# Kernel tuning notes

Measured on AMD Instinct MI355X. Metric: run time of the kernel, lower is better.

## Reference

```python
import jax, jax.numpy as jnp
import numpy as np

B, T, D = 4, 2048, 1024
H = 16
DH = D // H

def setup_inputs() -> dict:
    key = jax.random.key(0)
    k1, k2, k3 = jax.random.split(key, 3)
    x = jax.random.normal(k1, (B, T, D), dtype=jnp.float32)
    causal_mask = jnp.tril(jnp.ones((T, T), dtype=bool))[None, None]  # (1,1,T,T)
    Wqkv = jax.random.normal(k2, (D, 3 * D), dtype=jnp.float32) * (1.0 / np.sqrt(D))
    Wout = jax.random.normal(k3, (D, D), dtype=jnp.float32) * (1.0 / np.sqrt(D))
    return {"x": x, "causal_mask": causal_mask, "Wqkv": Wqkv, "Wout": Wout}

def reference(x, causal_mask, Wqkv, Wout):
    Bb, Tt, C = x.shape
    scale = jnp.sqrt(jnp.asarray(DH, dtype=x.dtype))
    qkv = x @ Wqkv                                   # (B,T,3D)
    qkv = qkv.reshape(Bb, Tt, 3, H, DH)
    qkv = jnp.transpose(qkv, (2, 0, 3, 1, 4))        # (3,B,H,T,DH)
    q, k, v = qkv[0], qkv[1], qkv[2]
    attn = jnp.einsum('bhqd,bhkd->bhqk', q, k) / scale
    attn = jnp.where(causal_mask, attn, jnp.asarray(-jnp.inf, dtype=attn.dtype))
    attn = jax.nn.softmax(attn, axis=-1)             # dropout p=0 -> identity
    out = jnp.einsum('bhqk,bhkd->bhqd', attn, v)     # (B,H,T,DH)
    out = jnp.transpose(out, (0, 2, 1, 3)).reshape(Bb, Tt, C)
    return out @ Wout
```

## Files before the change

kernel.cpp:

```cpp
#include <hip/hip_runtime.h>
#include <hip/hip_bf16.h>
#include <math.h>


#define Bb 4
#define Tt 2048
#define Dd 1024
#define Hh 16
#define DH 64
#define Mrows (Bb*Tt)
#define NEGBIG (-1.0e30f)
#define KB64 (Dd/64)
#define CHUNKS 1024
#define TILEU16 8192

typedef unsigned short u16;
typedef __attribute__((ext_vector_type(8))) short bf16x8;
typedef __attribute__((ext_vector_type(4))) float f32x4;

__device__ __forceinline__ u16 f2bf(float f) {
    union { float f; unsigned int i; } v; v.f = f;
    unsigned int x = v.i;
    return (u16)((x + 0x7fffu + ((x >> 16) & 1u)) >> 16);
}

__device__ __forceinline__ unsigned int cvt_pk_bf16(float lo, float hi) {
    unsigned int r;
    asm("v_cvt_pk_bf16_f32 %0, %1, %2" : "=v"(r) : "v"(lo), "v"(hi));
    return r;
}

__device__ __forceinline__ float exp2_(float x) {
#if __has_builtin(__builtin_amdgcn_exp2f)
    return __builtin_amdgcn_exp2f(x);
#else
    return __expf(x * 0.69314718056f);
#endif
}

typedef __attribute__((address_space(1))) const void glob_cv;
typedef __attribute__((address_space(3))) void lds_v;
__device__ __forceinline__ void gl2lds16(const void* g, void* l) {
    __builtin_amdgcn_global_load_lds((glob_cv*)g, (lds_v*)l, 16, 0, 0);
}

__global__ __launch_bounds__(256) void convert_x_tiled(const float* __restrict__ src,
                                                       u16* __restrict__ dst) {
    const int mb = blockIdx.x >> 4, kb = blockIdx.x & 15;
    const int row = threadIdx.x & 127, half = threadIdx.x >> 7;
    const float* s = src + (size_t)(mb * 128 + row) * Dd + kb * 64 + half * 32;
    u16* base = dst + (size_t)blockIdx.x * TILEU16;
    #pragma unroll
    for (int cq = 0; cq < 4; ++cq) {
        const int kq = half * 4 + cq;
        float4 f0 = *(const float4*)(s + cq * 8);
        float4 f1 = *(const float4*)(s + cq * 8 + 4);
        uint4 o;
        o.x = cvt_pk_bf16(f0.x, f0.y); o.y = cvt_pk_bf16(f0.z, f0.w);
        o.z = cvt_pk_bf16(f1.x, f1.y); o.w = cvt_pk_bf16(f1.z, f1.w);
        *(uint4*)(base + (size_t)(kq * 128 + row) * 8) = o;
    }
}

__global__ __launch_bounds__(256) void convert_w_tiled(const float* __restrict__ W,
                                                       u16* __restrict__ Wt,
                                                       int N) {
    __shared__ u16 t[128][68];
    const int nb = blockIdx.x, kb = blockIdx.y;
    const int k0 = kb * 64, n0 = nb * 128;
    const int k = threadIdx.x >> 2, ng = threadIdx.x & 3;
    const float* s = W + (size_t)(k0 + k) * N + n0 + ng * 32;
    #pragma unroll
    for (int i = 0; i < 8; ++i) {
        float4 f = *(const float4*)(s + i * 4);
        const int n = ng * 32 + i * 4;
        t[n + 0][k] = f2bf(f.x); t[n + 1][k] = f2bf(f.y);
        t[n + 2][k] = f2bf(f.z); t[n + 3][k] = f2bf(f.w);
    }
    __syncthreads();
    u16* base = Wt + (size_t)(nb * KB64 + kb) * TILEU16;
    #pragma unroll
    for (int it = 0; it < 4; ++it) {
        const int c = it * 256 + threadIdx.x;
        const int row = c & 127, kq = c >> 7;
        union { u16 u[8]; uint4 v; } o;
        #pragma unroll
        for (int j = 0; j < 8; ++j) o.u[j] = t[row][kq * 8 + j];
        *(uint4*)(base + (size_t)c * 8) = o.v;
    }
}

template <int MODE>
__global__ __launch_bounds__(256) void gemm_mfma(const u16* __restrict__ At,
                                                 const u16* __restrict__ Bt,
                                                 u16* __restrict__ Qo,
                                                 u16* __restrict__ KT,
                                                 u16* __restrict__ VtT,
                                                 float* __restrict__ Out) {
    __shared__ u16 As[8 * 128 * 8];
    __shared__ u16 Bs[8 * 128 * 8];
    const int tid  = threadIdx.x;
    const int lane = tid & 63, w = tid >> 6;
    const int ml   = lane & 15, q = lane >> 4;
    const int wm   = w >> 1, wn = w & 1;
    const int m0 = blockIdx.y * 128;

    const u16* Abase = At + (size_t)blockIdx.y * KB64 * TILEU16;
    const u16* Bbase = Bt + (size_t)blockIdx.x * KB64 * TILEU16;

    f32x4 acc[4][4];
    #pragma unroll
    for (int i = 0; i < 4; ++i)
        #pragma unroll
        for (int j = 0; j < 4; ++j) acc[i][j] = (f32x4){0.f, 0.f, 0.f, 0.f};

    for (int kb = 0; kb < KB64; ++kb) {
        __syncthreads();
        const u16* Ak = Abase + (size_t)kb * TILEU16;
        const u16* Bk = Bbase + (size_t)kb * TILEU16;
        #pragma unroll
        for (int it = 0; it < 4; ++it) {
            const int c = it * 256 + tid;
            gl2lds16(Ak + (size_t)c * 8, (char*)As + c * 16);
            gl2lds16(Bk + (size_t)c * 8, (char*)Bs + c * 16);
        }
        __syncthreads();

        #pragma unroll
        for (int ks = 0; ks < 2; ++ks) {
            const int kq = ks * 4 + q;
            bf16x8 af[4], bfr[4];
            #pragma unroll
            for (int i = 0; i < 4; ++i)
                af[i] = *(const bf16x8*)((const char*)As +
                        ((kq * 128) + wm * 64 + i * 16 + ml) * 16);
            #pragma unroll
            for (int j = 0; j < 4; ++j)
                bfr[j] = *(const bf16x8*)((const char*)Bs +
                        ((kq * 128) + wn * 64 + j * 16 + ml) * 16);
            #pragma unroll
            for (int i = 0; i < 4; ++i)
                #pragma unroll
                for (int j = 0; j < 4; ++j)
                    acc[i][j] = __builtin_amdgcn_mfma_f32_16x16x32_bf16(
                            bfr[j], af[i], acc[i][j], 0, 0, 0);
        }
    }

    if (MODE == 0) {
        const int s  = (blockIdx.x * 128) >> 10;
        const int h0 = ((blockIdx.x * 128) & 1023) >> 6;
        #pragma unroll
        for (int i = 0; i < 4; ++i) {
            const int m  = m0 + wm * 64 + i * 16 + ml;
            const int bb = m >> 11, t = m & 2047;
            const int bhn = bb * Hh + h0 + wn;
            #pragma unroll
            for (int j = 0; j < 4; ++j) {
                const int dh = j * 16 + q * 4;
                if (s == 2) {
                    u16* vb = VtT + (size_t)(bhn * 16 + (t >> 7)) * TILEU16;
                    #pragma unroll
                    for (int r = 0; r < 4; ++r)
                        vb[(size_t)(((t >> 3) & 15) * 64 + dh + r) * 8 + (t & 7)]
                            = f2bf(acc[i][j][r]);
                } else if (s == 1) {
                    uint2 pk;
                    pk.x = cvt_pk_bf16(acc[i][j][0], acc[i][j][1]);
                    pk.y = cvt_pk_bf16(acc[i][j][2], acc[i][j][3]);
                    *(uint2*)(KT + (size_t)(bhn * 16 + (t >> 7)) * TILEU16 +
                              (size_t)((j * 2 + (q >> 1)) * 128 + (t & 127)) * 8 +
                              (q & 1) * 4) = pk;
                } else {
                    const float sc = 0.125f * 1.44269504089f;
                    uint2 pk;
                    pk.x = cvt_pk_bf16(acc[i][j][0] * sc, acc[i][j][1] * sc);
                    pk.y = cvt_pk_bf16(acc[i][j][2] * sc, acc[i][j][3] * sc);
                    *(uint2*)(Qo + ((size_t)bhn * Tt + t) * DH + dh) = pk;
                }
            }
        }
    } else {
        #pragma unroll
        for (int i = 0; i < 4; ++i) {
            const int m = m0 + wm * 64 + i * 16 + ml;
            #pragma unroll
            for (int j = 0; j < 4; ++j) {
                const int n = blockIdx.x * 128 + wn * 64 + j * 16 + q * 4;
                float4 st = {acc[i][j][0], acc[i][j][1], acc[i][j][2], acc[i][j][3]};
                *(float4*)(Out + (size_t)m * Dd + n) = st;
            }
        }
    }
}

__device__ __forceinline__ void softmax_pv(f32x4 (&st)[8], float& m_i, float& l_i,
                                           f32x4 (&accO)[4], char* PsW,
                                           const char* VsBuf, int nl, int q,
                                           int qrow, bool diag) {
    if (diag) {
        #pragma unroll
        for (int kt = 0; kt < 8; ++kt)
            #pragma unroll
            for (int r = 0; r < 4; ++r)
                if (kt * 16 + q * 4 + r > qrow) st[kt][r] = NEGBIG;
    }
    float mx = NEGBIG;
    #pragma unroll
    for (int kt = 0; kt < 8; ++kt) {
        float a0 = fmaxf(st[kt][0], st[kt][1]);
        float a1 = fmaxf(st[kt][2], st[kt][3]);
        mx = fmaxf(fmaxf(mx, a0), a1);
    }
    mx = fmaxf(mx, __shfl_xor(mx, 16, 64));
    mx = fmaxf(mx, __shfl_xor(mx, 32, 64));

    float nm = m_i;
    if (__any(mx > m_i + 8.f)) {
        nm = fmaxf(m_i, mx);
        const float alpha = exp2_(m_i - nm);
        m_i = nm;
        l_i *= alpha;
        #pragma unroll
        for (int dt = 0; dt < 4; ++dt)
            #pragma unroll
            for (int r = 0; r < 4; ++r) accO[dt][r] *= alpha;
    }

    float rs = 0.f;
    #pragma unroll
    for (int kt = 0; kt < 8; ++kt) {
        const float p0 = exp2_(st[kt][0] - nm);
        const float p1 = exp2_(st[kt][1] - nm);
        const float p2 = exp2_(st[kt][2] - nm);
        const float p3 = exp2_(st[kt][3] - nm);
        rs += (p0 + p1) + (p2 + p3);
        uint2 pk;
        pk.x = cvt_pk_bf16(p0, p1);
        pk.y = cvt_pk_bf16(p2, p3);
        *(uint2*)(PsW + nl * 272 + kt * 32 + q * 8) = pk;
    }
    rs += __shfl_xor(rs, 16, 64);
    rs += __shfl_xor(rs, 32, 64);
    l_i += rs;

    __builtin_amdgcn_s_setprio(1);
    #pragma unroll
    for (int s = 0; s < 4; ++s) {
        bf16x8 bp = *(const bf16x8*)(PsW + nl * 272 + s * 64 + q * 16);
        #pragma unroll
        for (int dt = 0; dt < 4; ++dt) {
            bf16x8 av = *(const bf16x8*)(VsBuf +
                    ((s * 4 + q) * 64 + dt * 16 + nl) * 16);
            accO[dt] = __builtin_amdgcn_mfma_f32_16x16x32_bf16(
                    av, bp, accO[dt], 0, 0, 0);
        }
    }
    __builtin_amdgcn_s_setprio(0);
}

__global__ __launch_bounds__(256, 2) void attn_mfma(const u16* __restrict__ Q,
                                                    const u16* __restrict__ KT,
                                                    const u16* __restrict__ VtT,
                                                    u16* __restrict__ AOT) {
    __shared__ u16 Ks[8 * 128 * 8];
    __shared__ u16 Vs[2][16 * 64 * 8];
    __shared__ u16 Ps[4][16 * 136];

    const int tid  = threadIdx.x;
    const int lane = tid & 63, w = tid >> 6;
    const int nl   = lane & 15, q = lane >> 4;
    const int bh = blockIdx.y, b = bh >> 4, h = bh & 15;
    const size_t kbase = (size_t)bh * Tt * DH;

    for (int phase = 0; phase < 2; ++phase) {
        const int qt = phase ? (15 - (int)blockIdx.x) : (int)blockIdx.x;
        const int q0 = qt * 128;
        const int nj = (q0 >> 7) + 1;

        bf16x8 qf[2][2];
        #pragma unroll
        for (int qb = 0; qb < 2; ++qb)
            #pragma unroll
            for (int s = 0; s < 2; ++s)
                qf[qb][s] = *(const bf16x8*)(Q + kbase +
                        (size_t)(q0 + w * 32 + qb * 16 + nl) * DH + (s * 4 + q) * 8);

        float m_i[2] = {NEGBIG, NEGBIG};
        float l_i[2] = {0.f, 0.f};
        f32x4 accO[2][4];
        #pragma unroll
        for (int qb = 0; qb < 2; ++qb)
            #pragma unroll
            for (int dt = 0; dt < 4; ++dt) accO[qb][dt] = (f32x4){0.f, 0.f, 0.f, 0.f};

        __syncthreads();
        {
            const u16* Kb = KT  + (size_t)(bh * 16) * TILEU16;
            const u16* Vb = VtT + (size_t)(bh * 16) * TILEU16;
            #pragma unroll
            for (int it = 0; it < 4; ++it) {
                const int c = it * 256 + tid;
                gl2lds16(Kb + (size_t)c * 8, (char*)Ks + c * 16);
                gl2lds16(Vb + (size_t)c * 8, (char*)Vs[0] + c * 16);
            }
        }

        for (int jt = 0; jt < nj; ++jt) {
            const int buf = jt & 1;
            __syncthreads();

            f32x4 st0[8], st1[8];
            #pragma unroll
            for (int kt = 0; kt < 8; ++kt) {
                st0[kt] = (f32x4){0.f, 0.f, 0.f, 0.f};
                st1[kt] = (f32x4){0.f, 0.f, 0.f, 0.f};
            }
            __builtin_amdgcn_s_setprio(1);
            #pragma unroll
            for (int s = 0; s < 2; ++s) {
                #pragma unroll
                for (int kt = 0; kt < 8; ++kt) {
                    bf16x8 ak = *(const bf16x8*)((const char*)Ks +
                            ((s * 4 + q) * 128 + kt * 16 + nl) * 16);
                    st0[kt] = __builtin_amdgcn_mfma_f32_16x16x32_bf16(
                            ak, qf[0][s], st0[kt], 0, 0, 0);
                    st1[kt] = __builtin_amdgcn_mfma_f32_16x16x32_bf16(
                            ak, qf[1][s], st1[kt], 0, 0, 0);
                }
            }
            __builtin_amdgcn_s_setprio(0);

            __syncthreads();

            if (jt + 1 < nj) {
                const u16* Kb = KT  + (size_t)(bh * 16 + jt + 1) * TILEU16;
                const u16* Vb = VtT + (size_t)(bh * 16 + jt + 1) * TILEU16;
                #pragma unroll
                for (int it = 0; it < 4; ++it) {
                    const int c = it * 256 + tid;
                    gl2lds16(Kb + (size_t)c * 8, (char*)Ks + c * 16);
                    gl2lds16(Vb + (size_t)c * 8, (char*)Vs[buf ^ 1] + c * 16);
                }
            }

            const bool diag = (jt == nj - 1);
            softmax_pv(st0, m_i[0], l_i[0], accO[0], (char*)Ps[w],
                       (const char*)Vs[buf], nl, q, w * 32 + 0 * 16 + nl, diag);
            softmax_pv(st1, m_i[1], l_i[1], accO[1], (char*)Ps[w],
                       (const char*)Vs[buf], nl, q, w * 32 + 1 * 16 + nl, diag);
        }

        #pragma unroll
        for (int qb = 0; qb < 2; ++qb) {
            const float inv = 1.0f / l_i[qb];
            const int t = q0 + w * 32 + qb * 16 + nl;
            const int m = b * Tt + t;
            u16* ab = AOT + (size_t)((m >> 7) * KB64 + h) * TILEU16;
            #pragma unroll
            for (int dt = 0; dt < 4; ++dt) {
                uint2 pk;
                pk.x = cvt_pk_bf16(accO[qb][dt][0] * inv, accO[qb][dt][1] * inv);
                pk.y = cvt_pk_bf16(accO[qb][dt][2] * inv, accO[qb][dt][3] * inv);
                *(uint2*)(ab + (size_t)((dt * 2 + (q >> 1)) * 128 + (m & 127)) * 8 +
                          (q & 1) * 4) = pk;
            }
        }
    }
}

extern "C" void kernel_launch(void* const* d_in, const int* in_sizes, int n_in,
                              void* d_out, int out_size, void* d_ws, size_t ws_size,
                              hipStream_t stream) {
    const float* x_raw    = (const float*)d_in[0];
    const float* Wqkv_raw = (const float*)d_in[2];
    const float* Wout_raw = (const float*)d_in[3];
    float* out = (float*)d_out;

    const size_t SZ = (size_t)Bb * Hh * Tt * DH;
    u16* ws = (u16*)d_ws;
    u16* Qw     = ws;
    u16* KT     = ws + SZ;
    u16* VtT    = ws + 2 * SZ;
    u16* AOT    = ws + 3 * SZ;
    u16* WqkvT  = ws + 4 * SZ;
    u16* WoutT  = WqkvT + (size_t)3 * Dd * Dd;
    u16* xT     = (u16*)d_out;

    convert_x_tiled<<<dim3(64 * KB64), 256, 0, stream>>>(x_raw, xT);
    convert_w_tiled<<<dim3(3 * Dd / 128, KB64), 256, 0, stream>>>(Wqkv_raw, WqkvT, 3 * Dd);
    convert_w_tiled<<<dim3(Dd / 128, KB64),     256, 0, stream>>>(Wout_raw, WoutT, Dd);

    gemm_mfma<0><<<dim3(3 * Dd / 128, Mrows / 128), 256, 0, stream>>>(xT, WqkvT, Qw, KT, VtT, nullptr);
    attn_mfma  <<<dim3(Tt / 256, Bb * Hh), 256, 0, stream>>>(Qw, KT, VtT, AOT);
    gemm_mfma<1><<<dim3(Dd / 128, Mrows / 128), 256, 0, stream>>>(AOT, WoutT, nullptr, nullptr, nullptr, out);
}
```

Before: 279.1 us.

## Build P operand in registers via permlane swaps, drop LDS P staging

The softmax probabilities are packed into bf16 registers and rearranged into the MFMA B-operand layout with v_permlane32/16_swap, so the per-warp LDS round trip for P goes away. The two query sub-blocks' PV MFMAs are also interleaved. Each block now handles one 128-row query tile, with heaviest tiles first, instead of looping over a paired light and heavy tile. The grid doubles to 16x64 and launch bounds rise to 3 blocks per CU. This relies on the permlane swap giving the right lane layout, and adds register pressure and a less even load per block.

```diff
diff --git a/kernel.cpp b/kernel.cpp
--- a/kernel.cpp
+++ b/kernel.cpp
@@ -17,6 +17,7 @@
 typedef unsigned short u16;
 typedef __attribute__((ext_vector_type(8))) short bf16x8;
 typedef __attribute__((ext_vector_type(4))) float f32x4;
+typedef __attribute__((ext_vector_type(4))) unsigned int u32x4;
 
 __device__ __forceinline__ u16 f2bf(float f) {
     union { float f; unsigned int i; } v; v.f = f;
@@ -28,6 +29,13 @@
     unsigned int r;
     asm("v_cvt_pk_bf16_f32 %0, %1, %2" : "=v"(r) : "v"(lo), "v"(hi));
     return r;
+}
+
+__device__ __forceinline__ void perm32swap(unsigned& x, unsigned& y) {
+    asm("v_permlane32_swap_b32 %0, %1" : "+v"(x), "+v"(y));
+}
+__device__ __forceinline__ void perm16swap(unsigned& x, unsigned& y) {
+    asm("v_permlane16_swap_b32 %0, %1" : "+v"(x), "+v"(y));
 }
 
 __device__ __forceinline__ float exp2_(float x) {
@@ -194,10 +202,10 @@
     }
 }
 
-__device__ __forceinline__ void softmax_pv(f32x4 (&st)[8], float& m_i, float& l_i,
-                                           f32x4 (&accO)[4], char* PsW,
-                                           const char* VsBuf, int nl, int q,
-                                           int qrow, bool diag) {
+__device__ __forceinline__ void softmax_pack(f32x4 (&st)[8], float& m_i, float& l_i,
+                                             f32x4 (&accO)[4], unsigned (&d)[8],
+                                             unsigned (&e)[8], int q, int qrow,
+                                             bool diag) {
     if (diag) {
         #pragma unroll
         for (int kt = 0; kt < 8; ++kt)
@@ -235,37 +243,31 @@
         const float p2 = exp2_(st[kt][2] - nm);
         const float p3 = exp2_(st[kt][3] - nm);
         rs += (p0 + p1) + (p2 + p3);
-        uint2 pk;
-        pk.x = cvt_pk_bf16(p0, p1);
-        pk.y = cvt_pk_bf16(p2, p3);
-        *(uint2*)(PsW + nl * 272 + kt * 32 + q * 8) = pk;
+        d[kt] = cvt_pk_bf16(p0, p1);
+        e[kt] = cvt_pk_bf16(p2, p3);
     }
     rs += __shfl_xor(rs, 16, 64);
     rs += __shfl_xor(rs, 32, 64);
     l_i += rs;
-
-    __builtin_amdgcn_s_setprio(1);
-    #pragma unroll
-    for (int s = 0; s < 4; ++s) {
-        bf16x8 bp = *(const bf16x8*)(PsW + nl * 272 + s * 64 + q * 16);
-        #pragma unroll
-        for (int dt = 0; dt < 4; ++dt) {
-            bf16x8 av = *(const bf16x8*)(VsBuf +
-                    ((s * 4 + q) * 64 + dt * 16 + nl) * 16);
-            accO[dt] = __builtin_amdgcn_mfma_f32_16x16x32_bf16(
-                    av, bp, accO[dt], 0, 0, 0);
-        }
-    }
-    __builtin_amdgcn_s_setprio(0);
-}
-
-__global__ __launch_bounds__(256, 2) void attn_mfma(const u16* __restrict__ Q,
+}
+
+__device__ __forceinline__ bf16x8 build_bp(const unsigned (&d)[8],
+                                           const unsigned (&e)[8], int s) {
+    unsigned w0 = d[2 * s], w2 = d[2 * s + 1];
+    perm32swap(w0, w2); perm16swap(w0, w2);
+    unsigned w1 = e[2 * s], w3 = e[2 * s + 1];
+    perm32swap(w1, w3); perm16swap(w1, w3);
+    union { u32x4 u; bf16x8 b; } cv;
+    cv.u = (u32x4){w0, w1, w2, w3};
+    return cv.b;
+}
+
+__global__ __launch_bounds__(256, 3) void attn_mfma(const u16* __restrict__ Q,
                                                     const u16* __restrict__ KT,
                                                     const u16* __restrict__ VtT,
                                                     u16* __restrict__ AOT) {
     __shared__ u16 Ks[8 * 128 * 8];
     __shared__ u16 Vs[2][16 * 64 * 8];
-    __shared__ u16 Ps[4][16 * 136];
 
     const int tid  = threadIdx.x;
     const int lane = tid & 63, w = tid >> 6;
@@ -273,98 +275,111 @@
     const int bh = blockIdx.y, b = bh >> 4, h = bh & 15;
     const size_t kbase = (size_t)bh * Tt * DH;
 
-    for (int phase = 0; phase < 2; ++phase) {
-        const int qt = phase ? (15 - (int)blockIdx.x) : (int)blockIdx.x;
-        const int q0 = qt * 128;
-        const int nj = (q0 >> 7) + 1;
-
-        bf16x8 qf[2][2];
-        #pragma unroll
-        for (int qb = 0; qb < 2; ++qb)
-            #pragma unroll
-            for (int s = 0; s < 2; ++s)
-                qf[qb][s] = *(const bf16x8*)(Q + kbase +
-                        (size_t)(q0 + w * 32 + qb * 16 + nl) * DH + (s * 4 + q) * 8);
-
-        float m_i[2] = {NEGBIG, NEGBIG};
-        float l_i[2] = {0.f, 0.f};
-        f32x4 accO[2][4];
-        #pragma unroll
-        for (int qb = 0; qb < 2; ++qb)
-            #pragma unroll
-            for (int dt = 0; dt < 4; ++dt) accO[qb][dt] = (f32x4){0.f, 0.f, 0.f, 0.f};
-
+    const int qt = 15 - (int)blockIdx.x;
+    const int q0 = qt * 128;
+    const int nj = qt + 1;
+
+    bf16x8 qf[2][2];
+    #pragma unroll
+    for (int qb = 0; qb < 2; ++qb)
+        #pragma unroll
+        for (int s = 0; s < 2; ++s)
+            qf[qb][s] = *(const bf16x8*)(Q + kbase +
+                    (size_t)(q0 + w * 32 + qb * 16 + nl) * DH + (s * 4 + q) * 8);
+
+    float m_i[2] = {NEGBIG, NEGBIG};
+    float l_i[2] = {0.f, 0.f};
+    f32x4 accO[2][4];
+    #pragma unroll
+    for (int qb = 0; qb < 2; ++qb)
+        #pragma unroll
+        for (int dt = 0; dt < 4; ++dt) accO[qb][dt] = (f32x4){0.f, 0.f, 0.f, 0.f};
+
+    {
+        const u16* Kb = KT  + (size_t)(bh * 16) * TILEU16;
+        const u16* Vb = VtT + (size_t)(bh * 16) * TILEU16;
+        #pragma unroll
+        for (int it = 0; it < 4; ++it) {
+            const int c = it * 256 + tid;
+            gl2lds16(Kb + (size_t)c * 8, (char*)Ks + c * 16);
+            gl2lds16(Vb + (size_t)c * 8, (char*)Vs[0] + c * 16);
+        }
+    }
+
+    for (int jt = 0; jt < nj; ++jt) {
+        const int buf = jt & 1;
         __syncthreads();
-        {
-            const u16* Kb = KT  + (size_t)(bh * 16) * TILEU16;
-            const u16* Vb = VtT + (size_t)(bh * 16) * TILEU16;
+
+        f32x4 st0[8], st1[8];
+        #pragma unroll
+        for (int kt = 0; kt < 8; ++kt) {
+            st0[kt] = (f32x4){0.f, 0.f, 0.f, 0.f};
+            st1[kt] = (f32x4){0.f, 0.f, 0.f, 0.f};
+        }
+        __builtin_amdgcn_s_setprio(1);
+        #pragma unroll
+        for (int s = 0; s < 2; ++s) {
+            #pragma unroll
+            for (int kt = 0; kt < 8; ++kt) {
+                bf16x8 ak = *(const bf16x8*)((const char*)Ks +
+                        ((s * 4 + q) * 128 + kt * 16 + nl) * 16);
+                st0[kt] = __builtin_amdgcn_mfma_f32_16x16x32_bf16(
+                        ak, qf[0][s], st0[kt], 0, 0, 0);
+                st1[kt] = __builtin_amdgcn_mfma_f32_16x16x32_bf16(
+                        ak, qf[1][s], st1[kt], 0, 0, 0);
+            }
+        }
+        __builtin_amdgcn_s_setprio(0);
+
+        __syncthreads();
+
+        if (jt + 1 < nj) {
+            const u16* Kb = KT  + (size_t)(bh * 16 + jt + 1) * TILEU16;
+            const u16* Vb = VtT + (size_t)(bh * 16 + jt + 1) * TILEU16;
             #pragma unroll
             for (int it = 0; it < 4; ++it) {
                 const int c = it * 256 + tid;
                 gl2lds16(Kb + (size_t)c * 8, (char*)Ks + c * 16);
-                gl2lds16(Vb + (size_t)c * 8, (char*)Vs[0] + c * 16);
+                gl2lds16(Vb + (size_t)c * 8, (char*)Vs[buf ^ 1] + c * 16);
             }
         }
 
-        for (int jt = 0; jt < nj; ++jt) {
-            const int buf = jt & 1;
-            __syncthreads();
-
-            f32x4 st0[8], st1[8];
-            #pragma unroll
-            for (int kt = 0; kt < 8; ++kt) {
-                st0[kt] = (f32x4){0.f, 0.f, 0.f, 0.f};
-                st1[kt] = (f32x4){0.f, 0.f, 0.f, 0.f};
+        const bool diag = (jt == nj - 1);
+        unsigned d0[8], e0[8], d1[8], e1[8];
+        softmax_pack(st0, m_i[0], l_i[0], accO[0], d0, e0, q, w * 32 + nl, diag);
+        softmax_pack(st1, m_i[1], l_i[1], accO[1], d1, e1, q, w * 32 + 16 + nl, diag);
+
+        __builtin_amdgcn_s_setprio(1);
+        #pragma unroll
+        for (int s = 0; s < 4; ++s) {
+            bf16x8 bp0 = build_bp(d0, e0, s);
+            bf16x8 bp1 = build_bp(d1, e1, s);
+            #pragma unroll
+            for (int dt = 0; dt < 4; ++dt) {
+                bf16x8 av = *(const bf16x8*)((const char*)Vs[buf] +
+                        ((s * 4 + q) * 64 + dt * 16 + nl) * 16);
+                accO[0][dt] = __builtin_amdgcn_mfma_f32_16x16x32_bf16(
+                        av, bp0, accO[0][dt], 0, 0, 0);
+                accO[1][dt] = __builtin_amdgcn_mfma_f32_16x16x32_bf16(
+                        av, bp1, accO[1][dt], 0, 0, 0);
             }
-            __builtin_amdgcn_s_setprio(1);
-            #pragma unroll
-            for (int s = 0; s < 2; ++s) {
-                #pragma unroll
-                for (int kt = 0; kt < 8; ++kt) {
-                    bf16x8 ak = *(const bf16x8*)((const char*)Ks +
-                            ((s * 4 + q) * 128 + kt * 16 + nl) * 16);
-                    st0[kt] = __builtin_amdgcn_mfma_f32_16x16x32_bf16(
-                            ak, qf[0][s], st0[kt], 0, 0, 0);
-                    st1[kt] = __builtin_amdgcn_mfma_f32_16x16x32_bf16(
-                            ak, qf[1][s], st1[kt], 0, 0, 0);
-                }
-            }
-            __builtin_amdgcn_s_setprio(0);
-
-            __syncthreads();
-
-            if (jt + 1 < nj) {
-                const u16* Kb = KT  + (size_t)(bh * 16 + jt + 1) * TILEU16;
-                const u16* Vb = VtT + (size_t)(bh * 16 + jt + 1) * TILEU16;
-                #pragma unroll
-                for (int it = 0; it < 4; ++it) {
-                    const int c = it * 256 + tid;
-                    gl2lds16(Kb + (size_t)c * 8, (char*)Ks + c * 16);
-                    gl2lds16(Vb + (size_t)c * 8, (char*)Vs[buf ^ 1] + c * 16);
-                }
-            }
-
-            const bool diag = (jt == nj - 1);
-            softmax_pv(st0, m_i[0], l_i[0], accO[0], (char*)Ps[w],
-                       (const char*)Vs[buf], nl, q, w * 32 + 0 * 16 + nl, diag);
-            softmax_pv(st1, m_i[1], l_i[1], accO[1], (char*)Ps[w],
-                       (const char*)Vs[buf], nl, q, w * 32 + 1 * 16 + nl, diag);
-        }
-
-        #pragma unroll
-        for (int qb = 0; qb < 2; ++qb) {
-            const float inv = 1.0f / l_i[qb];
-            const int t = q0 + w * 32 + qb * 16 + nl;
-            const int m = b * Tt + t;
-            u16* ab = AOT + (size_t)((m >> 7) * KB64 + h) * TILEU16;
-            #pragma unroll
-            for (int dt = 0; dt < 4; ++dt) {
-                uint2 pk;
-                pk.x = cvt_pk_bf16(accO[qb][dt][0] * inv, accO[qb][dt][1] * inv);
-                pk.y = cvt_pk_bf16(accO[qb][dt][2] * inv, accO[qb][dt][3] * inv);
-                *(uint2*)(ab + (size_t)((dt * 2 + (q >> 1)) * 128 + (m & 127)) * 8 +
-                          (q & 1) * 4) = pk;
-            }
+        }
+        __builtin_amdgcn_s_setprio(0);
+    }
+
+    #pragma unroll
+    for (int qb = 0; qb < 2; ++qb) {
+        const float inv = 1.0f / l_i[qb];
+        const int t = q0 + w * 32 + qb * 16 + nl;
+        const int m = b * Tt + t;
+        u16* ab = AOT + (size_t)((m >> 7) * KB64 + h) * TILEU16;
+        #pragma unroll
+        for (int dt = 0; dt < 4; ++dt) {
+            uint2 pk;
+            pk.x = cvt_pk_bf16(accO[qb][dt][0] * inv, accO[qb][dt][1] * inv);
+            pk.y = cvt_pk_bf16(accO[qb][dt][2] * inv, accO[qb][dt][3] * inv);
+            *(uint2*)(ab + (size_t)((dt * 2 + (q >> 1)) * 128 + (m & 127)) * 8 +
+                      (q & 1) * 4) = pk;
         }
     }
 }
@@ -392,6 +407,6 @@
     convert_w_tiled<<<dim3(Dd / 128, KB64),     256, 0, stream>>>(Wout_raw, WoutT, Dd);
 
     gemm_mfma<0><<<dim3(3 * Dd / 128, Mrows / 128), 256, 0, stream>>>(xT, WqkvT, Qw, KT, VtT, nullptr);
-    attn_mfma  <<<dim3(Tt / 256, Bb * Hh), 256, 0, stream>>>(Qw, KT, VtT, AOT);
+    attn_mfma  <<<dim3(16, Bb * Hh), 256, 0, stream>>>(Qw, KT, VtT, AOT);
     gemm_mfma<1><<<dim3(Dd / 128, Mrows / 128), 256, 0, stream>>>(AOT, WoutT, nullptr, nullptr, nullptr, out);
 }
```

New measurement: 303.5 us. +8.7%, slower.
